# Kernel optimization log

Measured on AMD Instinct MI355X. Metric: run time of the kernel, lower is better.

The kernel has to match this reference:

```python
import jax, jax.numpy as jnp
import numpy as np

B, DIM, H, W = 32, 384, 32, 32
ORDER = 5
DIMS = [DIM // 2**i for i in range(ORDER)][::-1]  # [24,48,96,192,384]
SUM_DIMS = sum(DIMS)                               # 744 == 2*DIM - DIMS[0]
SCALE = 1.0 / 3.0
EPS = 1e-5


def setup_inputs() -> dict:
    key = jax.random.key(0)
    ks = jax.random.split(key, 32)

    def n(k, shape, s=0.02):
        return jax.random.normal(k, shape, jnp.float32) * s

    inp = {}
    inp['x'] = jax.random.normal(ks[0], (B, DIM, H, W), jnp.float32)
    # norm1: LayerNorm([dim, H, W]) -> per-element affine
    inp['ln1_w'] = jnp.ones((DIM, H, W), jnp.float32) + n(ks[1], (DIM, H, W))
    inp['ln1_b'] = n(ks[2], (DIM, H, W))
    # gnconv params
    inp['proj_in_w'] = n(ks[3], (2 * DIM, DIM))   # 1x1 conv stored as [O,C]
    inp['proj_in_b'] = n(ks[4], (2 * DIM,))
    inp['dw_w'] = n(ks[5], (SUM_DIMS, 1, 7, 7))   # depthwise 7x7
    inp['dw_b'] = n(ks[6], (SUM_DIMS,))
    for i in range(ORDER - 1):
        inp[f'pw{i}_w'] = n(ks[7 + 2 * i], (DIMS[i + 1], DIMS[i]))
        inp[f'pw{i}_b'] = n(ks[8 + 2 * i], (DIMS[i + 1],))
    inp['proj_out_w'] = n(ks[15], (DIM, DIM))
    inp['proj_out_b'] = n(ks[16], (DIM,))
    # norm2 + MLP
    inp['ln2_w'] = jnp.ones((DIM,), jnp.float32) + n(ks[17], (DIM,))
    inp['ln2_b'] = n(ks[18], (DIM,))
    inp['fc1_w'] = n(ks[19], (4 * DIM, DIM))
    inp['fc1_b'] = n(ks[20], (4 * DIM,))
    inp['fc2_w'] = n(ks[21], (DIM, 4 * DIM))
    inp['fc2_b'] = n(ks[22], (DIM,))
    # layer scales
    inp['gamma1'] = 1e-6 * jnp.ones((DIM,), jnp.float32)
    inp['gamma2'] = 1e-6 * jnp.ones((DIM,), jnp.float32)
    return inp


def _conv1x1(x, w, b):
    # x: [B,C,H,W], w: [O,C] -> [B,O,H,W]
    return jnp.einsum('bchw,oc->bohw', x, w) + b[None, :, None, None]


def _dwconv7(x, w, b):
    y = jax.lax.conv_general_dilated(
        x, w, window_strides=(1, 1), padding=[(3, 3), (3, 3)],
        dimension_numbers=('NCHW', 'OIHW', 'NCHW'),
        feature_group_count=x.shape[1])
    return y + b[None, :, None, None]


def reference(x, ln1_w, ln1_b, proj_in_w, proj_in_b, dw_w, dw_b,
              pw0_w, pw0_b, pw1_w, pw1_b, pw2_w, pw2_b, pw3_w, pw3_b,
              proj_out_w, proj_out_b, ln2_w, ln2_b,
              fc1_w, fc1_b, fc2_w, fc2_b, gamma1, gamma2):
    # ---- norm1: LayerNorm over (C,H,W) jointly ----
    mu = x.mean(axis=(1, 2, 3), keepdims=True)
    var = x.var(axis=(1, 2, 3), keepdims=True)
    h = (x - mu) * jax.lax.rsqrt(var + EPS) * ln1_w[None] + ln1_b[None]

    # ---- gnconv (recursive gated conv) ----
    fused = _conv1x1(h, proj_in_w, proj_in_b)          # [B, 2*DIM, H, W]
    pwa = fused[:, :DIMS[0]]
    abc = fused[:, DIMS[0]:]                            # [B, SUM_DIMS, H, W]
    dw = _dwconv7(abc, dw_w, dw_b) * SCALE
    dw_list = jnp.split(dw, np.cumsum(DIMS)[:-1].tolist(), axis=1)
    y = pwa * dw_list[0]
    for i, (wp, bp) in enumerate([(pw0_w, pw0_b), (pw1_w, pw1_b), (pw2_w, pw2_b), (pw3_w, pw3_b)]):
        y = _conv1x1(y, wp, bp) * dw_list[i + 1]
    y = _conv1x1(y, proj_out_w, proj_out_b)             # [B, DIM, H, W]

    x = x + gamma1[None, :, None, None] * y             # residual 1 (drop_path=0 -> identity)

    # ---- ConvNeXt-style MLP, channels-last ----
    h = jnp.transpose(x, (0, 2, 3, 1))                  # [B,H,W,C]
    mu2 = h.mean(axis=-1, keepdims=True)
    var2 = h.var(axis=-1, keepdims=True)
    h = (h - mu2) * jax.lax.rsqrt(var2 + EPS) * ln2_w + ln2_b
    h = jnp.einsum('bhwc,oc->bhwo', h, fc1_w) + fc1_b
    h = jax.nn.gelu(h, approximate=False)               # torch GELU default = erf
    h = jnp.einsum('bhwc,oc->bhwo', h, fc2_w) + fc2_b
    h = gamma2 * h
    h = jnp.transpose(h, (0, 3, 1, 2))                  # back to NCHW
    return x + h
```

## Files before the change

kernel.cpp:

```cpp
#include <hip/hip_runtime.h>
#include <math.h>

#define HW 1024
#define CDIM 384
#define NB 32
#define MTOT (NB * HW)
#define EPS 1e-5f

typedef unsigned short u16;
typedef short s8v __attribute__((ext_vector_type(8)));
typedef short s4v __attribute__((ext_vector_type(4)));
typedef float f4v __attribute__((ext_vector_type(4)));

union U8 { s8v v; u16 u[8]; };

__device__ __forceinline__ float bf2f(u16 u) {
  union { float f; unsigned int i; } x; x.i = ((unsigned int)u) << 16; return x.f;
}
__device__ __forceinline__ u16 f2bf(float f) {
  union { float f; unsigned int i; } x; x.f = f;
  unsigned int r = (x.i + 0x7FFFu + ((x.i >> 16) & 1u)) >> 16;
  return (u16)r;
}
__device__ __forceinline__ float gelu_exact(float v) {
  return 0.5f * v * (1.f + erff(v * 0.70710678118654752f));
}

__device__ __forceinline__ void gload16(const u16* g, u16* l) {
  __builtin_amdgcn_global_load_lds(
      (const __attribute__((address_space(1))) unsigned int*)(unsigned long long)(const void*)g,
      (__attribute__((address_space(3))) unsigned int*)(unsigned int)(unsigned long long)(void*)l,
      16, 0, 0);
}

__global__ __launch_bounds__(256) void k_statsA(const float* __restrict__ x,
                                                float* __restrict__ part) {
  int blk = blockIdx.x;
  const float4* xb = (const float4*)(x + (size_t)blk * 12288);
  float s = 0.f, s2 = 0.f;
  for (int i = threadIdx.x; i < 3072; i += 256) {
    float4 v = xb[i];
    s += v.x + v.y + v.z + v.w;
    s2 += v.x * v.x + v.y * v.y + v.z * v.z + v.w * v.w;
  }
  __shared__ float ls[256], ls2[256];
  ls[threadIdx.x] = s; ls2[threadIdx.x] = s2;
  __syncthreads();
  for (int off = 128; off > 0; off >>= 1) {
    if (threadIdx.x < off) {
      ls[threadIdx.x] += ls[threadIdx.x + off];
      ls2[threadIdx.x] += ls2[threadIdx.x + off];
    }
    __syncthreads();
  }
  if (threadIdx.x == 0) { part[blk * 2] = ls[0]; part[blk * 2 + 1] = ls2[0]; }
}

__global__ void k_statsB(const float* __restrict__ part, float* __restrict__ stats) {
  int b = threadIdx.x;
  if (b >= 32) return;
  float s = 0.f, s2 = 0.f;
  for (int i = 0; i < 32; i++) {
    s += part[(b * 32 + i) * 2];
    s2 += part[(b * 32 + i) * 2 + 1];
  }
  const float inv_n = 1.f / (CDIM * HW);
  float m = s * inv_n;
  stats[b] = m;
  stats[32 + b] = rsqrtf(s2 * inv_n - m * m + EPS);
}

__global__ __launch_bounds__(256) void k_cvtwE(const float* __restrict__ piw,
                                               const float* __restrict__ pow_,
                                               const float* __restrict__ p0w,
                                               const float* __restrict__ p1w,
                                               const float* __restrict__ p2w,
                                               const float* __restrict__ p3w,
                                               u16* __restrict__ dst) {
  int i = blockIdx.x * 256 + threadIdx.x;
  if (i < 294912) dst[i] = f2bf(piw[i]);
  else if (i < 442368) dst[i] = f2bf(pow_[i - 294912]);
  else if (i < 443904) { int j = i - 442368, o = j >> 5, k = j & 31;
    dst[i] = (k < 24) ? f2bf(p0w[o * 24 + k]) : (u16)0; }
  else if (i < 450048) { int j = i - 443904, o = j >> 6, k = j & 63;
    dst[i] = (k < 48) ? f2bf(p1w[o * 48 + k]) : (u16)0; }
  else if (i < 468480) dst[i] = f2bf(p2w[i - 450048]);
  else dst[i] = f2bf(p3w[i - 468480]);
}

__global__ __launch_bounds__(256) void k_cvtwL(const float* __restrict__ fc1,
                                               const float* __restrict__ fc2,
                                               u16* __restrict__ dst) {
  int i = blockIdx.x * 256 + threadIdx.x;
  if (i < 589824) dst[i] = f2bf(fc1[i]);
  else dst[i] = f2bf(fc2[i - 589824]);
}

__global__ __launch_bounds__(256) void k_trln1(const float* __restrict__ x,
                                               const float* __restrict__ lnw,
                                               const float* __restrict__ lnb,
                                               const float* __restrict__ stats,
                                               u16* __restrict__ xn,
                                               u16* __restrict__ hn) {
  int pt = blockIdx.x, ct = blockIdx.y, b = blockIdx.z;
  __shared__ float xs[32][33], hs[32][33];
  float m = stats[b], rs = stats[32 + b];
  int t = threadIdx.x;
  int ci0 = t >> 5, pi = t & 31;
#pragma unroll
  for (int it = 0; it < 4; it++) {
    int ci = ci0 + it * 8;
    int c = ct * 32 + ci;
    size_t src = ((size_t)b * CDIM + c) * HW + pt * 32 + pi;
    size_t wsrc = (size_t)c * HW + pt * 32 + pi;
    float xv = x[src];
    xs[ci][pi] = xv;
    hs[ci][pi] = (xv - m) * rs * lnw[wsrc] + lnb[wsrc];
  }
  __syncthreads();
  int co = t & 31, pr0 = t >> 5;
#pragma unroll
  for (int it = 0; it < 4; it++) {
    int pr = pr0 + it * 8;
    int p = pt * 32 + pr;
    int c = ct * 32 + co;
    size_t dst = ((size_t)b * HW + p) * CDIM + c;
    xn[dst] = f2bf(xs[co][pr]);
    hn[dst] = f2bf(hs[co][pr]);
  }
}

template <int MODE>
__global__ __launch_bounds__(256)
void k_mfma(const u16* __restrict__ A, const u16* __restrict__ Wb,
            const float* __restrict__ bias, void* __restrict__ Out,
            const u16* __restrict__ gate, int gate_off,
            const u16* __restrict__ resbf, const float* __restrict__ gvec,
            int m_base, int K, int O, int OS) {
  __shared__ u16 As[4096];
  __shared__ u16 Bs[4096];
  const int t = threadIdx.x;
  const int m0 = blockIdx.x * 128, o0 = blockIdx.y * 128;
  const int w = t >> 6, l = t & 63;
  const int wm = (w >> 1) * 64, wn = (w & 1) * 64;
  const int lr = l & 15, lk = (l >> 4) * 8;

  const u16* gA = A + (size_t)(m0 + w * 32 + (l >> 2)) * K + (l & 3) * 8;
  const u16* gB = Wb + (size_t)(o0 + w * 32 + (l >> 2)) * K + (l & 3) * 8;
  u16* ldsA0 = As + w * 1024;
  u16* ldsB0 = Bs + w * 1024;

  f4v acc[4][4];
#pragma unroll
  for (int i = 0; i < 4; i++)
#pragma unroll
    for (int j = 0; j < 4; j++) acc[i][j] = {};

  for (int k0 = 0; k0 < K; k0 += 32) {
    gload16(gA + k0, ldsA0);
    gload16(gA + 16 * K + k0, ldsA0 + 512);
    gload16(gB + k0, ldsB0);
    gload16(gB + 16 * K + k0, ldsB0 + 512);
    __syncthreads();
    s8v a[4], b[4];
#pragma unroll
    for (int mi = 0; mi < 4; mi++)
      a[mi] = *(const s8v*)&As[(wm + mi * 16 + lr) * 32 + lk];
#pragma unroll
    for (int fj = 0; fj < 4; fj++)
      b[fj] = *(const s8v*)&Bs[(wn + fj * 16 + lr) * 32 + lk];
#pragma unroll
    for (int mi = 0; mi < 4; mi++)
#pragma unroll
      for (int fj = 0; fj < 4; fj++)
        acc[mi][fj] = __builtin_amdgcn_mfma_f32_16x16x32_bf16(a[mi], b[fj], acc[mi][fj], 0, 0, 0);
    __syncthreads();
  }

  const int orow = (l >> 4) * 4;
#pragma unroll
  for (int mi = 0; mi < 4; mi++) {
    int p = m0 + wm + mi * 16 + orow;
#pragma unroll
    for (int fj = 0; fj < 4; fj++) {
      int o = o0 + wn + fj * 16 + lr;
      if (MODE == 1 && o >= OS) continue;
      float bo = (MODE == 1 && o >= O) ? 0.f : bias[o];
      float gv = (MODE == 2 || MODE == 4) ? gvec[o] : 0.f;
      if (MODE == 4) {
        int gp = m_base + p;
        float4 st;
        float* stp = &st.x;
#pragma unroll
        for (int r = 0; r < 4; r++)
          stp[r] = bf2f(resbf[(size_t)(gp + r) * CDIM + o]) + gv * (acc[mi][fj][r] + bo);
        int bb = gp >> 10, hw = gp & 1023;
        *(float4*)((float*)Out + ((size_t)bb * CDIM + o) * HW + hw) = st;
      } else {
#pragma unroll
        for (int r = 0; r < 4; r++) {
          float val = acc[mi][fj][r] + bo;
          size_t rowi = (size_t)(p + r);
          if (MODE == 0) {
            ((u16*)Out)[rowi * OS + o] = f2bf(val);
          } else if (MODE == 1) {
            float g = (o < O) ? bf2f(gate[rowi * 744 + gate_off + o]) : 0.f;
            ((u16*)Out)[rowi * OS + o] = (o < O) ? f2bf(val * g) : (u16)0;
          } else if (MODE == 2) {
            size_t idx = rowi * CDIM + o;
            ((u16*)Out)[idx] = f2bf(bf2f(resbf[idx]) + gv * val);
          } else if (MODE == 3) {
            ((u16*)Out)[rowi * OS + o] = f2bf(gelu_exact(val));
          }
        }
      }
    }
  }
}

__global__ __launch_bounds__(256) void k_dwconv(const u16* __restrict__ fused,
                                                const float* __restrict__ w,
                                                const float* __restrict__ bias,
                                                u16* __restrict__ dwo,
                                                u16* __restrict__ y0) {
  const int ys = blockIdx.x;
  const int cb = blockIdx.y;
  const int b = blockIdx.z;
  __shared__ u16 tile[10][32][64];
  __shared__ float wk[64][49];
  const int c0 = cb * 64;
  const int t = threadIdx.x;
  for (int i = t; i < 64 * 49; i += 256) {
    int cc = i / 49, k = i % 49;
    wk[cc][k] = (c0 + cc < 744) ? w[(size_t)(c0 + cc) * 49 + k] : 0.f;
  }
  const int lx = t >> 3, lco = (t & 7) * 8;
  const int fch = 24 + c0 + lco;
#pragma unroll
  for (int yy = 0; yy < 10; yy++) {
    int y = ys * 4 - 3 + yy;
    s8v v = {0, 0, 0, 0, 0, 0, 0, 0};
    if (y >= 0 && y < 32 && fch < 768)
      v = *(const s8v*)(fused + ((size_t)b * HW + y * 32 + lx) * 768 + fch);
    *(s8v*)&tile[yy][lx][lco] = v;
  }
  __syncthreads();
  const int c = t & 63, dy = t >> 6;
  const bool valid = (c0 + c) < 744;
  const float bv = valid ? bias[c0 + c] : 0.f;
  float acc[32];
#pragma unroll
  for (int x = 0; x < 32; x++) acc[x] = 0.f;
#pragma unroll
  for (int ky = 0; ky < 7; ky++) {
    int yy = dy + ky;
    float r[38];
    r[0] = r[1] = r[2] = 0.f; r[35] = r[36] = r[37] = 0.f;
#pragma unroll
    for (int x = 0; x < 32; x++) r[x + 3] = bf2f(tile[yy][x][c]);
#pragma unroll
    for (int kx = 0; kx < 7; kx++) {
      float wv = wk[c][ky * 7 + kx];
#pragma unroll
      for (int x = 0; x < 32; x++) acc[x] += r[x + kx] * wv;
    }
  }
  const int yout = ys * 4 + dy;
  const size_t prow = (size_t)b * HW + yout * 32;
  if (valid) {
#pragma unroll
    for (int x = 0; x < 32; x++)
      dwo[(prow + x) * 744 + c0 + c] = f2bf((acc[x] + bv) * (1.f / 3.f));
  }
  if (cb == 0 && c < 32) {
#pragma unroll
    for (int x = 0; x < 32; x++) {
      u16 o = 0;
      if (c < 24)
        o = f2bf(bf2f(fused[(prow + x) * 768 + c]) * ((acc[x] + bv) * (1.f / 3.f)));
      y0[(prow + x) * 32 + c] = o;
    }
  }
}

__global__ __launch_bounds__(256) void k_ln2(const u16* __restrict__ xm,
                                             const float* __restrict__ w,
                                             const float* __restrict__ bb,
                                             u16* __restrict__ outp) {
  int row = blockIdx.x * 4 + (threadIdx.x >> 6);
  int l = threadIdx.x & 63;
  float v[8];
  float s = 0.f, s2 = 0.f;
  if (l < 48) {
    U8 u;
    u.v = *(const s8v*)(xm + (size_t)row * CDIM + l * 8);
#pragma unroll
    for (int i = 0; i < 8; i++) {
      v[i] = bf2f(u.u[i]);
      s += v[i]; s2 += v[i] * v[i];
    }
  }
#pragma unroll
  for (int off = 32; off > 0; off >>= 1) {
    s += __shfl_xor(s, off);
    s2 += __shfl_xor(s2, off);
  }
  const float inv_n = 1.f / CDIM;
  float m = s * inv_n;
  float rs = rsqrtf(s2 * inv_n - m * m + EPS);
  if (l < 48) {
    U8 res;
#pragma unroll
    for (int i = 0; i < 8; i++) {
      int c = l * 8 + i;
      res.u[i] = f2bf((v[i] - m) * rs * w[c] + bb[c]);
    }
    *(s8v*)(outp + (size_t)row * CDIM + l * 8) = res.v;
  }
}

extern "C" void kernel_launch(void* const* d_in, const int* in_sizes, int n_in,
                              void* d_out, int out_size, void* d_ws, size_t ws_size,
                              hipStream_t stream) {
  const float* x          = (const float*)d_in[0];
  const float* ln1_w      = (const float*)d_in[1];
  const float* ln1_b      = (const float*)d_in[2];
  const float* proj_in_w  = (const float*)d_in[3];
  const float* proj_in_b  = (const float*)d_in[4];
  const float* dw_w       = (const float*)d_in[5];
  const float* dw_b       = (const float*)d_in[6];
  const float* pw0_w      = (const float*)d_in[7];
  const float* pw0_b      = (const float*)d_in[8];
  const float* pw1_w      = (const float*)d_in[9];
  const float* pw1_b      = (const float*)d_in[10];
  const float* pw2_w      = (const float*)d_in[11];
  const float* pw2_b      = (const float*)d_in[12];
  const float* pw3_w      = (const float*)d_in[13];
  const float* pw3_b      = (const float*)d_in[14];
  const float* proj_out_w = (const float*)d_in[15];
  const float* proj_out_b = (const float*)d_in[16];
  const float* ln2_w      = (const float*)d_in[17];
  const float* ln2_b      = (const float*)d_in[18];
  const float* fc1_w      = (const float*)d_in[19];
  const float* fc1_b      = (const float*)d_in[20];
  const float* fc2_w      = (const float*)d_in[21];
  const float* fc2_b      = (const float*)d_in[22];
  const float* gamma1     = (const float*)d_in[23];
  const float* gamma2     = (const float*)d_in[24];
  float* out = (float*)d_out;

  const size_t MiB = 1ull << 20;
  char* ws = (char*)d_ws;
  u16* xn   = (u16*)(ws + 0);
  u16* hn   = (u16*)(ws + 24 * MiB);
  u16* fus  = (u16*)(ws + 48 * MiB);
  u16* dw   = (u16*)(ws + 96 * MiB);
  u16* wE   = (u16*)(ws + 142 * MiB + 512 * 1024);
  float* stats = (float*)(ws + 143 * MiB + 768 * 1024);
  float* part  = stats + 64;
  u16* y0 = (u16*)(ws + 24 * MiB);
  u16* y1 = (u16*)(ws + 26 * MiB);
  u16* y2 = (u16*)(ws + 30 * MiB);
  u16* y3 = (u16*)(ws + 36 * MiB);
  u16* y4 = (u16*)(ws + 48 * MiB);
  u16* xmid = (u16*)(ws + 72 * MiB);
  u16* ln2h = (u16*)(ws + 0);
  u16* fc1b = (u16*)(ws + 24 * MiB);
  u16* fc2b = fc1b + 589824;
  u16* h1 = (u16*)(ws + 96 * MiB);

  u16* piw_b = wE;
  u16* pow_b = wE + 294912;
  u16* pw0b  = wE + 442368;
  u16* pw1b  = wE + 443904;
  u16* pw2b  = wE + 450048;
  u16* pw3b  = wE + 468480;

  k_statsA<<<1024, 256, 0, stream>>>(x, part);
  k_statsB<<<1, 64, 0, stream>>>(part, stats);
  k_cvtwE<<<2118, 256, 0, stream>>>(proj_in_w, proj_out_w, pw0_w, pw1_w, pw2_w, pw3_w, wE);
  k_trln1<<<dim3(32, 12, NB), 256, 0, stream>>>(x, ln1_w, ln1_b, stats, xn, hn);
  k_mfma<0><<<dim3(256, 6), 256, 0, stream>>>(hn, piw_b, proj_in_b, fus, nullptr, 0,
                                              nullptr, nullptr, 0, 384, 768, 768);
  k_dwconv<<<dim3(8, 12, NB), 256, 0, stream>>>(fus, dw_w, dw_b, dw, y0);
  k_mfma<1><<<dim3(256, 1), 256, 0, stream>>>(y0, pw0b, pw0_b, y1, dw, 24, nullptr,
                                              nullptr, 0, 32, 48, 64);
  k_mfma<1><<<dim3(256, 1), 256, 0, stream>>>(y1, pw1b, pw1_b, y2, dw, 72, nullptr,
                                              nullptr, 0, 64, 96, 96);
  k_mfma<1><<<dim3(256, 2), 256, 0, stream>>>(y2, pw2b, pw2_b, y3, dw, 168, nullptr,
                                              nullptr, 0, 96, 192, 192);
  k_mfma<1><<<dim3(256, 3), 256, 0, stream>>>(y3, pw3b, pw3_b, y4, dw, 360, nullptr,
                                              nullptr, 0, 192, 384, 384);
  k_mfma<2><<<dim3(256, 3), 256, 0, stream>>>(y4, pow_b, proj_out_b, xmid, nullptr, 0,
                                              xn, gamma1, 0, 384, 384, 384);
  k_ln2<<<MTOT / 4, 256, 0, stream>>>(xmid, ln2_w, ln2_b, ln2h);
  k_cvtwL<<<4608, 256, 0, stream>>>(fc1_w, fc2_w, fc1b);
  for (int ch = 0; ch < 2; ch++) {
    int m_base = ch * 16384;
    k_mfma<3><<<dim3(128, 12), 256, 0, stream>>>(ln2h + (size_t)m_base * CDIM, fc1b,
                                                 fc1_b, h1, nullptr, 0, nullptr, nullptr,
                                                 0, 384, 1536, 1536);
    k_mfma<4><<<dim3(128, 3), 256, 0, stream>>>(h1, fc2b, fc2_b, out, nullptr, 0, xmid,
                                                gamma2, m_base, 1536, 384, 384);
  }
}
```

Measured before the change: 446.4 us.

## Double GEMM K-step per sync, coalesce dwconv weight load, split y0 into own kernel

The MFMA GEMM loop now stages two 32-wide K slices into doubled LDS buffers before each barrier pair, halving the number of __syncthreads per K and giving more loads in flight. The depthwise conv weight staging is reordered so consecutive threads read channel-strided addresses, and the pwa*dw0 gating that only block column 0 did is moved into a separate elementwise kernel. The change doubles shared memory per GEMM block, which may lower occupancy, and adds one extra launch plus a reread of dw.

```diff
diff --git a/kernel.cpp b/kernel.cpp
--- a/kernel.cpp
+++ b/kernel.cpp
@@ -9,7 +9,6 @@
 
 typedef unsigned short u16;
 typedef short s8v __attribute__((ext_vector_type(8)));
-typedef short s4v __attribute__((ext_vector_type(4)));
 typedef float f4v __attribute__((ext_vector_type(4)));
 
 union U8 { s8v v; u16 u[8]; };
@@ -137,8 +136,8 @@
             const u16* __restrict__ gate, int gate_off,
             const u16* __restrict__ resbf, const float* __restrict__ gvec,
             int m_base, int K, int O, int OS) {
-  __shared__ u16 As[4096];
-  __shared__ u16 Bs[4096];
+  __shared__ u16 As[8192];
+  __shared__ u16 Bs[8192];
   const int t = threadIdx.x;
   const int m0 = blockIdx.x * 128, o0 = blockIdx.y * 128;
   const int w = t >> 6, l = t & 63;
@@ -156,24 +155,47 @@
 #pragma unroll
     for (int j = 0; j < 4; j++) acc[i][j] = {};
 
-  for (int k0 = 0; k0 < K; k0 += 32) {
+  for (int k0 = 0; k0 < K; k0 += 64) {
+    const bool two = (k0 + 32 < K);
     gload16(gA + k0, ldsA0);
     gload16(gA + 16 * K + k0, ldsA0 + 512);
     gload16(gB + k0, ldsB0);
     gload16(gB + 16 * K + k0, ldsB0 + 512);
+    if (two) {
+      gload16(gA + k0 + 32, ldsA0 + 4096);
+      gload16(gA + 16 * K + k0 + 32, ldsA0 + 4096 + 512);
+      gload16(gB + k0 + 32, ldsB0 + 4096);
+      gload16(gB + 16 * K + k0 + 32, ldsB0 + 4096 + 512);
+    }
     __syncthreads();
-    s8v a[4], b[4];
-#pragma unroll
-    for (int mi = 0; mi < 4; mi++)
-      a[mi] = *(const s8v*)&As[(wm + mi * 16 + lr) * 32 + lk];
-#pragma unroll
-    for (int fj = 0; fj < 4; fj++)
-      b[fj] = *(const s8v*)&Bs[(wn + fj * 16 + lr) * 32 + lk];
-#pragma unroll
-    for (int mi = 0; mi < 4; mi++)
+    {
+      s8v a[4], b[4];
+#pragma unroll
+      for (int mi = 0; mi < 4; mi++)
+        a[mi] = *(const s8v*)&As[(wm + mi * 16 + lr) * 32 + lk];
 #pragma unroll
       for (int fj = 0; fj < 4; fj++)
-        acc[mi][fj] = __builtin_amdgcn_mfma_f32_16x16x32_bf16(a[mi], b[fj], acc[mi][fj], 0, 0, 0);
+        b[fj] = *(const s8v*)&Bs[(wn + fj * 16 + lr) * 32 + lk];
+#pragma unroll
+      for (int mi = 0; mi < 4; mi++)
+#pragma unroll
+        for (int fj = 0; fj < 4; fj++)
+          acc[mi][fj] = __builtin_amdgcn_mfma_f32_16x16x32_bf16(a[mi], b[fj], acc[mi][fj], 0, 0, 0);
+    }
+    if (two) {
+      s8v a[4], b[4];
+#pragma unroll
+      for (int mi = 0; mi < 4; mi++)
+        a[mi] = *(const s8v*)&As[4096 + (wm + mi * 16 + lr) * 32 + lk];
+#pragma unroll
+      for (int fj = 0; fj < 4; fj++)
+        b[fj] = *(const s8v*)&Bs[4096 + (wn + fj * 16 + lr) * 32 + lk];
+#pragma unroll
+      for (int mi = 0; mi < 4; mi++)
+#pragma unroll
+        for (int fj = 0; fj < 4; fj++)
+          acc[mi][fj] = __builtin_amdgcn_mfma_f32_16x16x32_bf16(a[mi], b[fj], acc[mi][fj], 0, 0, 0);
+    }
     __syncthreads();
   }
 
@@ -221,8 +243,7 @@
 __global__ __launch_bounds__(256) void k_dwconv(const u16* __restrict__ fused,
                                                 const float* __restrict__ w,
                                                 const float* __restrict__ bias,
-                                                u16* __restrict__ dwo,
-                                                u16* __restrict__ y0) {
+                                                u16* __restrict__ dwo) {
   const int ys = blockIdx.x;
   const int cb = blockIdx.y;
   const int b = blockIdx.z;
@@ -230,9 +251,9 @@
   __shared__ float wk[64][49];
   const int c0 = cb * 64;
   const int t = threadIdx.x;
-  for (int i = t; i < 64 * 49; i += 256) {
-    int cc = i / 49, k = i % 49;
-    wk[cc][k] = (c0 + cc < 744) ? w[(size_t)(c0 + cc) * 49 + k] : 0.f;
+  for (int i = t; i < 64 * 64; i += 256) {
+    int k = i >> 6, cc = i & 63;
+    if (k < 49) wk[cc][k] = (c0 + cc < 744) ? w[(size_t)(c0 + cc) * 49 + k] : 0.f;
   }
   const int lx = t >> 3, lco = (t & 7) * 8;
   const int fch = 24 + c0 + lco;
@@ -265,22 +286,22 @@
       for (int x = 0; x < 32; x++) acc[x] += r[x + kx] * wv;
     }
   }
-  const int yout = ys * 4 + dy;
-  const size_t prow = (size_t)b * HW + yout * 32;
   if (valid) {
+    const int yout = ys * 4 + dy;
+    const size_t prow = (size_t)b * HW + yout * 32;
 #pragma unroll
     for (int x = 0; x < 32; x++)
       dwo[(prow + x) * 744 + c0 + c] = f2bf((acc[x] + bv) * (1.f / 3.f));
   }
-  if (cb == 0 && c < 32) {
-#pragma unroll
-    for (int x = 0; x < 32; x++) {
-      u16 o = 0;
-      if (c < 24)
-        o = f2bf(bf2f(fused[(prow + x) * 768 + c]) * ((acc[x] + bv) * (1.f / 3.f)));
-      y0[(prow + x) * 32 + c] = o;
-    }
-  }
+}
+
+__global__ __launch_bounds__(256) void k_y0(const u16* __restrict__ fused,
+                                            const u16* __restrict__ dwo,
+                                            u16* __restrict__ y0) {
+  int i = blockIdx.x * 256 + threadIdx.x;
+  int p = i >> 5, c = i & 31;
+  y0[i] = (c < 24) ? f2bf(bf2f(fused[(size_t)p * 768 + c]) * bf2f(dwo[(size_t)p * 744 + c]))
+                   : (u16)0;
 }
 
 __global__ __launch_bounds__(256) void k_ln2(const u16* __restrict__ xm,
@@ -382,7 +403,8 @@
   k_trln1<<<dim3(32, 12, NB), 256, 0, stream>>>(x, ln1_w, ln1_b, stats, xn, hn);
   k_mfma<0><<<dim3(256, 6), 256, 0, stream>>>(hn, piw_b, proj_in_b, fus, nullptr, 0,
                                               nullptr, nullptr, 0, 384, 768, 768);
-  k_dwconv<<<dim3(8, 12, NB), 256, 0, stream>>>(fus, dw_w, dw_b, dw, y0);
+  k_dwconv<<<dim3(8, 12, NB), 256, 0, stream>>>(fus, dw_w, dw_b, dw);
+  k_y0<<<(MTOT * 32) / 256, 256, 0, stream>>>(fus, dw, y0);
   k_mfma<1><<<dim3(256, 1), 256, 0, stream>>>(y0, pw0b, pw0_b, y1, dw, 24, nullptr,
                                               nullptr, 0, 32, 48, 64);
   k_mfma<1><<<dim3(256, 1), 256, 0, stream>>>(y1, pw1b, pw1_b, y2, dw, 72, nullptr,
```

New measurement: 451.9 us. About the same (+1.2%).
